# Kernel tuning notes

Measured on AMD Instinct MI355X. Metric: run time of the kernel, lower is better.

Reference implementation:

```python
import jax, jax.numpy as jnp
import numpy as np

N = 8192
NFEAT = 64
OUT = 64


def setup_inputs() -> dict:
    key = jax.random.key(0)
    ks = jax.random.split(key, 7)
    A_stack = jax.random.uniform(ks[0], (N, N, 5), dtype=jnp.float32)
    feature = jax.random.normal(ks[1], (N, NFEAT), dtype=jnp.float32)
    weight_b = jax.random.uniform(ks[2], (5, 1), dtype=jnp.float32) * 0.1
    stdv1 = 1.0 / np.sqrt(OUT)
    W1 = jax.random.uniform(ks[3], (NFEAT, OUT), dtype=jnp.float32, minval=-stdv1, maxval=stdv1)
    b1 = jax.random.uniform(ks[4], (OUT,), dtype=jnp.float32, minval=-stdv1, maxval=stdv1)
    W2 = jax.random.uniform(ks[5], (OUT, OUT), dtype=jnp.float32, minval=-stdv1, maxval=stdv1)
    b2 = jax.random.uniform(ks[6], (OUT,), dtype=jnp.float32, minval=-stdv1, maxval=stdv1)
    return {"A_stack": A_stack, "feature": feature, "weight_b": weight_b,
            "W1": W1, "b1": b1, "W2": W2, "b2": b2}


def reference(A_stack, feature, weight_b, W1, b1, W2, b2):
    # Multiplex relation aggregation: weighted sum of 5 adjacency layers, then symmetrize.
    temp = jnp.einsum('ijk,kl->ij', A_stack, weight_b)  # [N, N]
    final_A = temp + temp.T
    # GCN layer 1: spmm(adj, X @ W1) + b1
    U1 = final_A @ (feature @ W1) + b1
    # GCN layer 2
    U2 = final_A @ (U1 @ W2) + b2
    return (U1 + U2) * 0.5
```

## Files before the change

### kernel.cpp

```cpp
#include <hip/hip_runtime.h>
#include <hip/hip_bf16.h>


#define NN 8192

typedef __attribute__((ext_vector_type(8))) short short8;
typedef __attribute__((ext_vector_type(8))) unsigned short u16x8;
typedef __attribute__((ext_vector_type(4))) unsigned short u16x4;
typedef __attribute__((ext_vector_type(4))) float f32x4;

static __device__ __forceinline__ unsigned short f2bf(float f) {
    unsigned u = __float_as_uint(f);
    u += 0x7FFFu + ((u >> 16) & 1u);
    return (unsigned short)(u >> 16);
}

#define GL16(gsrc, ldst) __builtin_amdgcn_global_load_lds( \
    (const __attribute__((address_space(1))) void*)(gsrc), \
    (__attribute__((address_space(3))) void*)(ldst), 16, 0, 0)

__global__ __launch_bounds__(256) void k_sym_build(
        const float* __restrict__ A, const float* __restrict__ wb,
        unsigned short* __restrict__ S) {
    __shared__ float Tt[64 * 65];

    int b = blockIdx.x;
    double disc = 66049.0 - 8.0 * (double)b;
    int bi = (int)((257.0 - sqrt(disc)) * 0.5);
    if (bi < 0) bi = 0; if (bi > 127) bi = 127;
    while (bi < 127 && (bi + 1) * (257 - (bi + 1)) / 2 <= b) ++bi;
    while (bi > 0 && bi * (257 - bi) / 2 > b) --bi;
    int bj = bi + (b - bi * (257 - bi) / 2);

    const float w0 = wb[0], w1 = wb[1], w2 = wb[2], w3 = wb[3], w4 = wb[4];
    int t = threadIdx.x;
    int qc = t & 15;
    int r0 = t >> 4;

    float t1[4][4];
    #pragma unroll
    for (int e = 0; e < 4; ++e) {
        int r = r0 + 16 * e;
        {
            const f32x4* p = (const f32x4*)(A +
                ((long long)(bi * 64 + r) * NN + bj * 64 + 4 * qc) * 5);
            f32x4 f0 = p[0], f1 = p[1], f2 = p[2], f3 = p[3], f4 = p[4];
            t1[e][0] = f0[0]*w0 + f0[1]*w1 + f0[2]*w2 + f0[3]*w3 + f1[0]*w4;
            t1[e][1] = f1[1]*w0 + f1[2]*w1 + f1[3]*w2 + f2[0]*w3 + f2[1]*w4;
            t1[e][2] = f2[2]*w0 + f2[3]*w1 + f3[0]*w2 + f3[1]*w3 + f3[2]*w4;
            t1[e][3] = f3[3]*w0 + f4[0]*w1 + f4[1]*w2 + f4[2]*w3 + f4[3]*w4;
        }
        {
            const f32x4* p = (const f32x4*)(A +
                ((long long)(bj * 64 + r) * NN + bi * 64 + 4 * qc) * 5);
            f32x4 f0 = p[0], f1 = p[1], f2 = p[2], f3 = p[3], f4 = p[4];
            Tt[r * 65 + 4*qc + 0] = f0[0]*w0 + f0[1]*w1 + f0[2]*w2 + f0[3]*w3 + f1[0]*w4;
            Tt[r * 65 + 4*qc + 1] = f1[1]*w0 + f1[2]*w1 + f1[3]*w2 + f2[0]*w3 + f2[1]*w4;
            Tt[r * 65 + 4*qc + 2] = f2[2]*w0 + f2[3]*w1 + f3[0]*w2 + f3[1]*w3 + f3[2]*w4;
            Tt[r * 65 + 4*qc + 3] = f3[3]*w0 + f4[0]*w1 + f4[1]*w2 + f4[2]*w3 + f4[3]*w4;
        }
    }
    __syncthreads();
    float sv[4][4];
    #pragma unroll
    for (int e = 0; e < 4; ++e) {
        int r = r0 + 16 * e;
        u16x4 o;
        #pragma unroll
        for (int q = 0; q < 4; ++q) {
            float v = t1[e][q] + Tt[(4*qc + q) * 65 + r];
            sv[e][q] = v;
            o[q] = f2bf(v);
        }
        *(u16x4*)(S + (long long)(bi * 64 + r) * NN + bj * 64 + 4 * qc) = o;
    }
    __syncthreads();
    #pragma unroll
    for (int e = 0; e < 4; ++e) {
        int r = r0 + 16 * e;
        #pragma unroll
        for (int q = 0; q < 4; ++q) Tt[r * 65 + 4*qc + q] = sv[e][q];
    }
    __syncthreads();
    if (bi != bj) {
        #pragma unroll
        for (int e = 0; e < 4; ++e) {
            int r = r0 + 16 * e;
            u16x4 o;
            #pragma unroll
            for (int q = 0; q < 4; ++q) o[q] = f2bf(Tt[(4*qc + q) * 65 + r]);
            *(u16x4*)(S + (long long)(bj * 64 + r) * NN + bi * 64 + 4 * qc) = o;
        }
    }
}

__global__ __launch_bounds__(256) void k_small_gemm_t(
        const float* __restrict__ X, const float* __restrict__ W,
        unsigned short* __restrict__ Yt) {
    __shared__ float Ys[64 * 65];
    int t = threadIdx.x, lane = t & 63, w = t >> 6;
    float wcol[64];
    #pragma unroll
    for (int k = 0; k < 64; ++k) wcol[k] = W[k * 64 + lane];
    int r0 = blockIdx.x * 64;
    for (int rr = 0; rr < 16; ++rr) {
        const f32x4* x = (const f32x4*)(X + (long long)(r0 + w * 16 + rr) * 64);
        float acc = 0.f;
        #pragma unroll
        for (int k4 = 0; k4 < 16; ++k4) {
            f32x4 xv = x[k4];
            acc += xv[0]*wcol[4*k4] + xv[1]*wcol[4*k4+1]
                 + xv[2]*wcol[4*k4+2] + xv[3]*wcol[4*k4+3];
        }
        Ys[lane * 65 + w * 16 + rr] = acc;
    }
    __syncthreads();
    int c = t >> 2, j0 = (t & 3) * 16;
    u16x8 o0, o1;
    #pragma unroll
    for (int q = 0; q < 8; ++q) {
        o0[q] = f2bf(Ys[c * 65 + j0 + q]);
        o1[q] = f2bf(Ys[c * 65 + j0 + 8 + q]);
    }
    *(u16x8*)(Yt + (long long)c * NN + r0 + j0) = o0;
    *(u16x8*)(Yt + (long long)c * NN + r0 + j0 + 8) = o1;
}

template<int FINAL>
__global__ __launch_bounds__(256) void k_gemm_skinny(
        const unsigned short* __restrict__ S,
        const unsigned short* __restrict__ Ht,
        const float* __restrict__ bias,
        const float* __restrict__ U1,
        float* __restrict__ Y) {
    __shared__ unsigned short Ts[2][16 * 128];
    __shared__ unsigned short Hs[2][64 * 128];
    int t = threadIdx.x, lane = t & 63, w = t >> 6;
    int i0 = blockIdx.x * 16;
    int r = lane & 15, kg = lane >> 4;

    int srow = t >> 4, sc = t & 15;
    int sbyte = (sc * 16) ^ ((srow & 7) << 4);
    const unsigned short* aSrc = S + (long long)(i0 + srow) * NN + (sbyte >> 1);
    const unsigned short* hSrc = Ht + (long long)srow * NN + (sbyte >> 1);
    char* tsDst0 = (char*)&Ts[0][0] + t * 16;
    char* tsDst1 = (char*)&Ts[1][0] + t * 16;
    char* hsDst0 = (char*)&Hs[0][0] + t * 16;
    char* hsDst1 = (char*)&Hs[1][0] + t * 16;

    f32x4 acc = {0.f, 0.f, 0.f, 0.f};

    GL16(aSrc, tsDst0);
    #pragma unroll
    for (int q = 0; q < 4; ++q)
        GL16(hSrc + (long long)q * 16 * NN, hsDst0 + q * 4096);
    __syncthreads();

    int cur = 0;
    for (int jt = 0; jt < NN; jt += 128) {
        if (jt + 128 < NN) {
            if (cur == 0) {
                GL16(aSrc + jt + 128, tsDst1);
                #pragma unroll
                for (int q = 0; q < 4; ++q)
                    GL16(hSrc + (long long)q * 16 * NN + jt + 128, hsDst1 + q * 4096);
            } else {
                GL16(aSrc + jt + 128, tsDst0);
                #pragma unroll
                for (int q = 0; q < 4; ++q)
                    GL16(hSrc + (long long)q * 16 * NN + jt + 128, hsDst0 + q * 4096);
            }
        }
        const char* tsB = (const char*)&Ts[cur][0];
        const char* hsB = (const char*)&Hs[cur][0];
        int hr = w * 16 + r;
        #pragma unroll
        for (int kk = 0; kk < 4; ++kk) {
            int xo = kk * 64 + kg * 16;
            short8 a = *(const short8*)(tsB + r * 256 + (xo ^ ((r & 7) << 4)));
            short8 bb = *(const short8*)(hsB + hr * 256 + (xo ^ ((r & 7) << 4)));
            acc = __builtin_amdgcn_mfma_f32_16x16x32_bf16(a, bb, acc, 0, 0, 0);
        }
        __syncthreads();
        cur ^= 1;
    }

    int f = w * 16 + r;
    float bv = bias[f];
    #pragma unroll
    for (int rr = 0; rr < 4; ++rr) {
        long long gi = (long long)(i0 + kg * 4 + rr) * 64 + f;
        float v = acc[rr] + bv;
        if (FINAL) v = 0.5f * (U1[gi] + v);
        Y[gi] = v;
    }
}

extern "C" void kernel_launch(void* const* d_in, const int* in_sizes, int n_in,
                              void* d_out, int out_size, void* d_ws, size_t ws_size,
                              hipStream_t stream) {
    const float* A    = (const float*)d_in[0];
    const float* feat = (const float*)d_in[1];
    const float* wb   = (const float*)d_in[2];
    const float* W1   = (const float*)d_in[3];
    const float* b1   = (const float*)d_in[4];
    const float* W2   = (const float*)d_in[5];
    const float* b2   = (const float*)d_in[6];
    float* out = (float*)d_out;

    const size_t szS = (size_t)NN * NN * 2;
    const size_t szH = (size_t)64 * NN * 2;
    char* p = (char*)d_ws;
    unsigned short* S   = (unsigned short*)p;
    unsigned short* H1t = (unsigned short*)(p + szS);
    unsigned short* H2t = (unsigned short*)(p + szS + szH);
    float*          U1  = (float*)(p + szS + 2 * szH);

    k_sym_build<<<8256, 256, 0, stream>>>(A, wb, S);
    k_small_gemm_t<<<128, 256, 0, stream>>>(feat, W1, H1t);
    k_gemm_skinny<0><<<512, 256, 0, stream>>>(S, H1t, b1, nullptr, U1);
    k_small_gemm_t<<<128, 256, 0, stream>>>(U1, W2, H2t);
    k_gemm_skinny<1><<<512, 256, 0, stream>>>(S, H2t, b2, U1, out);
}
```

Before: 445.3 us.

## Stage A rows through LDS for coalesced loads in symmetric build

Rewrites the symmetric-adjacency build kernel so each wave loads a full contiguous 1280-byte row segment of A with coalesced 16-byte loads, stages it in LDS and deinterleaves the 5 layers there, instead of each thread reading five strided f32x4 vectors. Both the tile and its transpose are kept in LDS (one row-major, one transposed), which removes a sync round and lets the outputs be written as 8-wide bf16 stores. The intent is better DRAM coalescing on the dominant 1.3 GB read. In exchange it adds more LDS traffic, a serial 16-iteration loop per wave with only 80 of 64 lanes' worth of work per row, and a larger LDS footprint that may lower occupancy.

Measured after the change: 496.7 us. 11.5% more time.

```diff
diff --git a/kernel.cpp b/kernel.cpp
--- a/kernel.cpp
+++ b/kernel.cpp
@@ -22,7 +22,9 @@
 __global__ __launch_bounds__(256) void k_sym_build(
         const float* __restrict__ A, const float* __restrict__ wb,
         unsigned short* __restrict__ S) {
-    __shared__ float Tt[64 * 65];
+    __shared__ float raw[4][336];
+    __shared__ float T1s[64 * 65];
+    __shared__ float T2t[64 * 65];
 
     int b = blockIdx.x;
     double disc = 66049.0 - 8.0 * (double)b;
@@ -33,63 +35,55 @@
     int bj = bi + (b - bi * (257 - bi) / 2);
 
     const float w0 = wb[0], w1 = wb[1], w2 = wb[2], w3 = wb[3], w4 = wb[4];
-    int t = threadIdx.x;
-    int qc = t & 15;
-    int r0 = t >> 4;
-
-    float t1[4][4];
-    #pragma unroll
-    for (int e = 0; e < 4; ++e) {
-        int r = r0 + 16 * e;
-        {
-            const f32x4* p = (const f32x4*)(A +
-                ((long long)(bi * 64 + r) * NN + bj * 64 + 4 * qc) * 5);
-            f32x4 f0 = p[0], f1 = p[1], f2 = p[2], f3 = p[3], f4 = p[4];
-            t1[e][0] = f0[0]*w0 + f0[1]*w1 + f0[2]*w2 + f0[3]*w3 + f1[0]*w4;
-            t1[e][1] = f1[1]*w0 + f1[2]*w1 + f1[3]*w2 + f2[0]*w3 + f2[1]*w4;
-            t1[e][2] = f2[2]*w0 + f2[3]*w1 + f3[0]*w2 + f3[1]*w3 + f3[2]*w4;
-            t1[e][3] = f3[3]*w0 + f4[0]*w1 + f4[1]*w2 + f4[2]*w3 + f4[3]*w4;
-        }
-        {
-            const f32x4* p = (const f32x4*)(A +
-                ((long long)(bj * 64 + r) * NN + bi * 64 + 4 * qc) * 5);
-            f32x4 f0 = p[0], f1 = p[1], f2 = p[2], f3 = p[3], f4 = p[4];
-            Tt[r * 65 + 4*qc + 0] = f0[0]*w0 + f0[1]*w1 + f0[2]*w2 + f0[3]*w3 + f1[0]*w4;
-            Tt[r * 65 + 4*qc + 1] = f1[1]*w0 + f1[2]*w1 + f1[3]*w2 + f2[0]*w3 + f2[1]*w4;
-            Tt[r * 65 + 4*qc + 2] = f2[2]*w0 + f2[3]*w1 + f3[0]*w2 + f3[1]*w3 + f3[2]*w4;
-            Tt[r * 65 + 4*qc + 3] = f3[3]*w0 + f4[0]*w1 + f4[1]*w2 + f4[2]*w3 + f4[3]*w4;
+    int t = threadIdx.x, lane = t & 63, w = t >> 6;
+
+    #pragma unroll
+    for (int half = 0; half < 2; ++half) {
+        int tr = half == 0 ? bi : bj;
+        int tc = half == 0 ? bj : bi;
+        for (int rr = 0; rr < 16; ++rr) {
+            int r = rr * 4 + w;
+            const f32x4* rowp = (const f32x4*)(A +
+                ((long long)(tr * 64 + r) * NN + tc * 64) * 5);
+            f32x4 c0 = rowp[lane];
+            f32x4 c1;
+            if (lane < 16) c1 = rowp[64 + lane];
+            *(f32x4*)&raw[w][lane * 4] = c0;
+            if (lane < 16) *(f32x4*)&raw[w][256 + lane * 4] = c1;
+            asm volatile("s_waitcnt lgkmcnt(0)" ::: "memory");
+            float a0 = raw[w][5 * lane + 0];
+            float a1 = raw[w][5 * lane + 1];
+            float a2 = raw[w][5 * lane + 2];
+            float a3 = raw[w][5 * lane + 3];
+            float a4 = raw[w][5 * lane + 4];
+            float tv = a0 * w0 + a1 * w1 + a2 * w2 + a3 * w3 + a4 * w4;
+            __builtin_amdgcn_wave_barrier();
+            if (half == 0) T1s[r * 65 + lane] = tv;
+            else           T2t[lane * 65 + r] = tv;
         }
     }
     __syncthreads();
-    float sv[4][4];
-    #pragma unroll
-    for (int e = 0; e < 4; ++e) {
-        int r = r0 + 16 * e;
-        u16x4 o;
-        #pragma unroll
-        for (int q = 0; q < 4; ++q) {
-            float v = t1[e][q] + Tt[(4*qc + q) * 65 + r];
-            sv[e][q] = v;
-            o[q] = f2bf(v);
-        }
-        *(u16x4*)(S + (long long)(bi * 64 + r) * NN + bj * 64 + 4 * qc) = o;
-    }
-    __syncthreads();
-    #pragma unroll
-    for (int e = 0; e < 4; ++e) {
-        int r = r0 + 16 * e;
-        #pragma unroll
-        for (int q = 0; q < 4; ++q) Tt[r * 65 + 4*qc + q] = sv[e][q];
-    }
-    __syncthreads();
+
+    #pragma unroll
+    for (int e = 0; e < 2; ++e) {
+        int i = (t >> 3) + 32 * e;
+        int j0 = (t & 7) * 8;
+        u16x8 o;
+        #pragma unroll
+        for (int q = 0; q < 8; ++q)
+            o[q] = f2bf(T1s[i * 65 + j0 + q] + T2t[i * 65 + j0 + q]);
+        *(u16x8*)(S + (long long)(bi * 64 + i) * NN + bj * 64 + j0) = o;
+    }
     if (bi != bj) {
         #pragma unroll
-        for (int e = 0; e < 4; ++e) {
-            int r = r0 + 16 * e;
-            u16x4 o;
+        for (int e = 0; e < 2; ++e) {
+            int i = (t >> 3) + 32 * e;
+            int j0 = (t & 7) * 8;
+            u16x8 o;
             #pragma unroll
-            for (int q = 0; q < 4; ++q) o[q] = f2bf(Tt[(4*qc + q) * 65 + r]);
-            *(u16x4*)(S + (long long)(bj * 64 + r) * NN + bi * 64 + 4 * qc) = o;
+            for (int q = 0; q < 8; ++q)
+                o[q] = f2bf(T1s[(j0 + q) * 65 + i] + T2t[(j0 + q) * 65 + i]);
+            *(u16x8*)(S + (long long)(bj * 64 + i) * NN + bi * 64 + j0) = o;
         }
     }
 }
```

## Fuse first adjacency GEMM into symmetric build with atomic accumulation

Applied to the files above, without the earlier changes.

Computes the first GCN aggregation (S @ H1) inside the symmetric-adjacency build kernel, using each 64x64 bf16 tile already staged in LDS. Both the tile and its transpose are multiplied with MFMA, and the partial results are accumulated into U1 with fp32 atomics after a memset. This removes a full pass that re-reads the 128MB S matrix. The b1 bias is folded into the second small GEMM and the final epilogue. The cost is many contended global atomics, per-element strided LDS gathers for the transposed operand, and non-deterministic summation order.

New measurement: 458.1 us. +2.9%, slower.

```diff
diff --git a/kernel.cpp b/kernel.cpp
--- a/kernel.cpp
+++ b/kernel.cpp
@@ -19,10 +19,13 @@
     (const __attribute__((address_space(1))) void*)(gsrc), \
     (__attribute__((address_space(3))) void*)(ldst), 16, 0, 0)
 
-__global__ __launch_bounds__(256) void k_sym_build(
+__global__ __launch_bounds__(256) void k_sym_fused(
         const float* __restrict__ A, const float* __restrict__ wb,
-        unsigned short* __restrict__ S) {
+        const unsigned short* __restrict__ H1t,
+        unsigned short* __restrict__ S,
+        float* __restrict__ U1) {
     __shared__ float Tt[64 * 65];
+    __shared__ unsigned short Sb[64 * 72];
 
     int b = blockIdx.x;
     double disc = 66049.0 - 8.0 * (double)b;
@@ -61,7 +64,6 @@
         }
     }
     __syncthreads();
-    float sv[4][4];
     #pragma unroll
     for (int e = 0; e < 4; ++e) {
         int r = r0 + 16 * e;
@@ -69,43 +71,88 @@
         #pragma unroll
         for (int q = 0; q < 4; ++q) {
             float v = t1[e][q] + Tt[(4*qc + q) * 65 + r];
-            sv[e][q] = v;
             o[q] = f2bf(v);
         }
         *(u16x4*)(S + (long long)(bi * 64 + r) * NN + bj * 64 + 4 * qc) = o;
-    }
-    __syncthreads();
-    #pragma unroll
-    for (int e = 0; e < 4; ++e) {
-        int r = r0 + 16 * e;
-        #pragma unroll
-        for (int q = 0; q < 4; ++q) Tt[r * 65 + 4*qc + q] = sv[e][q];
-    }
-    __syncthreads();
+        *(u16x4*)(&Sb[r * 72 + 4 * qc]) = o;
+    }
+    __syncthreads();
+
     if (bi != bj) {
         #pragma unroll
-        for (int e = 0; e < 4; ++e) {
-            int r = r0 + 16 * e;
-            u16x4 o;
-            #pragma unroll
-            for (int q = 0; q < 4; ++q) o[q] = f2bf(Tt[(4*qc + q) * 65 + r]);
-            *(u16x4*)(S + (long long)(bj * 64 + r) * NN + bi * 64 + 4 * qc) = o;
-        }
+        for (int e = 0; e < 2; ++e) {
+            int i = (t >> 3) + 32 * e;
+            int j0 = (t & 7) * 8;
+            u16x8 o;
+            #pragma unroll
+            for (int q = 0; q < 8; ++q) o[q] = Sb[(j0 + q) * 72 + i];
+            *(u16x8*)(S + (long long)(bj * 64 + i) * NN + bi * 64 + j0) = o;
+        }
+    }
+
+    int lane = t & 63, w = t >> 6;
+    int r = lane & 15, kg = lane >> 4;
+    {
+        f32x4 acc[4] = {{0,0,0,0},{0,0,0,0},{0,0,0,0},{0,0,0,0}};
+        #pragma unroll
+        for (int kk = 0; kk < 2; ++kk) {
+            short8 a = *(const short8*)(&Sb[(w * 16 + r) * 72 + kk * 32 + kg * 8]);
+            #pragma unroll
+            for (int nt = 0; nt < 4; ++nt) {
+                short8 bb = *(const short8*)(H1t +
+                    (long long)(nt * 16 + r) * NN + bj * 64 + kk * 32 + kg * 8);
+                acc[nt] = __builtin_amdgcn_mfma_f32_16x16x32_bf16(a, bb, acc[nt], 0, 0, 0);
+            }
+        }
+        #pragma unroll
+        for (int nt = 0; nt < 4; ++nt)
+            #pragma unroll
+            for (int rr = 0; rr < 4; ++rr)
+                atomicAdd(U1 + (long long)(bi * 64 + w * 16 + kg * 4 + rr) * 64
+                             + nt * 16 + r, acc[nt][rr]);
+    }
+    if (bi != bj) {
+        f32x4 acc[4] = {{0,0,0,0},{0,0,0,0},{0,0,0,0},{0,0,0,0}};
+        #pragma unroll
+        for (int kk = 0; kk < 2; ++kk) {
+            short8 a;
+            #pragma unroll
+            for (int j = 0; j < 8; ++j)
+                a[j] = (short)Sb[(kk * 32 + kg * 8 + j) * 72 + w * 16 + r];
+            #pragma unroll
+            for (int nt = 0; nt < 4; ++nt) {
+                short8 bb = *(const short8*)(H1t +
+                    (long long)(nt * 16 + r) * NN + bi * 64 + kk * 32 + kg * 8);
+                acc[nt] = __builtin_amdgcn_mfma_f32_16x16x32_bf16(a, bb, acc[nt], 0, 0, 0);
+            }
+        }
+        #pragma unroll
+        for (int nt = 0; nt < 4; ++nt)
+            #pragma unroll
+            for (int rr = 0; rr < 4; ++rr)
+                atomicAdd(U1 + (long long)(bj * 64 + w * 16 + kg * 4 + rr) * 64
+                             + nt * 16 + r, acc[nt][rr]);
     }
 }
 
 __global__ __launch_bounds__(256) void k_small_gemm_t(
         const float* __restrict__ X, const float* __restrict__ W,
+        const float* __restrict__ bias,
         unsigned short* __restrict__ Yt) {
     __shared__ float Ys[64 * 65];
     int t = threadIdx.x, lane = t & 63, w = t >> 6;
     float wcol[64];
     #pragma unroll
     for (int k = 0; k < 64; ++k) wcol[k] = W[k * 64 + lane];
+    float bw = 0.f;
+    if (bias) {
+        #pragma unroll
+        for (int k = 0; k < 64; ++k) bw += bias[k] * wcol[k];
+    }
     int r0 = blockIdx.x * 64;
     for (int rr = 0; rr < 16; ++rr) {
         const f32x4* x = (const f32x4*)(X + (long long)(r0 + w * 16 + rr) * 64);
-        float acc = 0.f;
+        float acc = bw;
         #pragma unroll
         for (int k4 = 0; k4 < 16; ++k4) {
             f32x4 xv = x[k4];
@@ -126,11 +173,11 @@
     *(u16x8*)(Yt + (long long)c * NN + r0 + j0 + 8) = o1;
 }
 
-template<int FINAL>
-__global__ __launch_bounds__(256) void k_gemm_skinny(
+__global__ __launch_bounds__(256) void k_gemm_final(
         const unsigned short* __restrict__ S,
         const unsigned short* __restrict__ Ht,
-        const float* __restrict__ bias,
+        const float* __restrict__ b1,
+        const float* __restrict__ b2,
         const float* __restrict__ U1,
         float* __restrict__ Y) {
     __shared__ unsigned short Ts[2][16 * 128];
@@ -186,13 +233,11 @@
     }
 
     int f = w * 16 + r;
-    float bv = bias[f];
+    float bv = b1[f] + b2[f];
     #pragma unroll
     for (int rr = 0; rr < 4; ++rr) {
         long long gi = (long long)(i0 + kg * 4 + rr) * 64 + f;
-        float v = acc[rr] + bv;
-        if (FINAL) v = 0.5f * (U1[gi] + v);
-        Y[gi] = v;
+        Y[gi] = 0.5f * (U1[gi] + acc[rr] + bv);
     }
 }
 
@@ -210,15 +255,16 @@
 
     const size_t szS = (size_t)NN * NN * 2;
     const size_t szH = (size_t)64 * NN * 2;
+    const size_t szU = (size_t)NN * 64 * 4;
     char* p = (char*)d_ws;
     unsigned short* S   = (unsigned short*)p;
     unsigned short* H1t = (unsigned short*)(p + szS);
     unsigned short* H2t = (unsigned short*)(p + szS + szH);
     float*          U1  = (float*)(p + szS + 2 * szH);
 
-    k_sym_build<<<8256, 256, 0, stream>>>(A, wb, S);
-    k_small_gemm_t<<<128, 256, 0, stream>>>(feat, W1, H1t);
-    k_gemm_skinny<0><<<512, 256, 0, stream>>>(S, H1t, b1, nullptr, U1);
-    k_small_gemm_t<<<128, 256, 0, stream>>>(U1, W2, H2t);
-    k_gemm_skinny<1><<<512, 256, 0, stream>>>(S, H2t, b2, U1, out);
-}
+    k_small_gemm_t<<<128, 256, 0, stream>>>(feat, W1, nullptr, H1t);
+    hipMemsetAsync(U1, 0, szU, stream);
+    k_sym_fused<<<8256, 256, 0, stream>>>(A, wb, H1t, S, U1);
+    k_small_gemm_t<<<128, 256, 0, stream>>>(U1, W2, b1, H2t);
+    k_gemm_final<<<512, 256, 0, stream>>>(S, H2t, b1, b2, U1, out);
+}
```
